# Kernel tuning notes

Measured on AMD Instinct MI355X. Metric: run time of the kernel, lower is better.

## Reference

```python
import jax, jax.numpy as jnp
import numpy as np

DIM = 512
EPS = 1e-8
LN_EPS = 1e-5


def _layernorm(x, g, b):
    mu = jnp.mean(x, axis=-1, keepdims=True)
    var = jnp.mean(jnp.square(x - mu), axis=-1, keepdims=True)
    return (x - mu) * jax.lax.rsqrt(var + LN_EPS) * g + b


def setup_inputs() -> dict:
    key = jax.random.key(0)
    ks = jax.random.split(key, 8)
    b, i, j, d = 8, 2048, 2048, DIM
    s = 1.0 / np.sqrt(d)
    return {
        "inputs": jax.random.normal(ks[0], (b, i, d), dtype=jnp.float32),
        "context": jax.random.normal(ks[1], (b, j, d), dtype=jnp.float32),
        "g_in": jnp.ones((d,), jnp.float32),
        "b_in": jnp.zeros((d,), jnp.float32),
        "g_ctx": jnp.ones((d,), jnp.float32),
        "b_ctx": jnp.zeros((d,), jnp.float32),
        "Wq": jax.random.uniform(ks[2], (d, d), jnp.float32, -s, s),
        "bq": jnp.zeros((d,), jnp.float32),
        "Wk": jax.random.uniform(ks[3], (d, d), jnp.float32, -s, s),
        "bk": jnp.zeros((d,), jnp.float32),
        "Wv": jax.random.uniform(ks[4], (d, d), jnp.float32, -s, s),
        "bv": jnp.zeros((d,), jnp.float32),
    }


def reference(inputs, context, g_in, b_in, g_ctx, b_ctx, Wq, bq, Wk, bk, Wv, bv):
    scale = DIM ** (-0.5)
    x = _layernorm(inputs, g_in, b_in)
    c = _layernorm(context, g_ctx, b_ctx)
    q = x @ Wq + bq          # [b,i,d]
    k = c @ Wk + bk          # [b,j,d]
    v = c @ Wv + bv          # [b,j,d]
    dots = jnp.einsum('bid,bjd->bij', q, k) * scale
    # NOTE: non-standard softmax over the QUERY axis (dim=1), then eps shift
    attn = jax.nn.softmax(dots, axis=1) + EPS
    # second renormalization over the KEY axis (dim=2)
    mean_attn = attn / (jnp.sum(attn, axis=2, keepdims=True) + EPS)
    updates = jnp.einsum('bjd,bij->bid', v, mean_attn)
    return updates
```

## Files before the change

kernel.cpp:

```cpp
#include <hip/hip_runtime.h>
#include <hip/hip_bf16.h>
#include <math.h>

#define EPSF 1e-8f
#define LN_EPSF 1e-5f
#define SCALE_QK 0.04419417382415922f

typedef unsigned short ushort_t;
typedef __bf16 bhalf;
typedef bhalf bhalf8 __attribute__((ext_vector_type(8)));
typedef float f32x4 __attribute__((ext_vector_type(4)));

__device__ __forceinline__ float b2f(ushort_t u) {
    return __uint_as_float((unsigned)u << 16);
}
__device__ __forceinline__ ushort_t f2b(float f) {
    unsigned x = __float_as_uint(f);
    return (ushort_t)((x + 0x7fffu + ((x >> 16) & 1u)) >> 16);
}
__device__ __forceinline__ void gload16(const ushort_t* g, ushort_t* l) {
    __builtin_amdgcn_global_load_lds(
        (const __attribute__((address_space(1))) unsigned int*)g,
        (__attribute__((address_space(3))) unsigned int*)l, 16, 0, 0);
}

__global__ __launch_bounds__(256) void ln_apply_kernel(
    const float* __restrict__ X1, const float* __restrict__ X2,
    const float* __restrict__ g1, const float* __restrict__ b1,
    const float* __restrict__ g2, const float* __restrict__ b2,
    ushort_t* __restrict__ O1, ushort_t* __restrict__ O2)
{
    const bool sec = blockIdx.y != 0;
    const float* X = sec ? X2 : X1;
    const float* g = sec ? g2 : g1;
    const float* b = sec ? b2 : b1;
    ushort_t* O = sec ? O2 : O1;
    const size_t base = (size_t)blockIdx.x * 512;
    const int t = threadIdx.x;
    float a = X[base + t];
    float c = X[base + t + 256];
    float s = a + c;
    float q = fmaf(a, a, c * c);
#pragma unroll
    for (int off = 32; off > 0; off >>= 1) {
        s += __shfl_down(s, off, 64);
        q += __shfl_down(q, off, 64);
    }
    __shared__ float ls[4], lq[4], mv[2];
    int lane = t & 63, w = t >> 6;
    if (lane == 0) { ls[w] = s; lq[w] = q; }
    __syncthreads();
    if (t == 0) {
        float st = ls[0] + ls[1] + ls[2] + ls[3];
        float qt = lq[0] + lq[1] + lq[2] + lq[3];
        float mu = st * (1.0f / 512.0f);
        float var = qt * (1.0f / 512.0f) - mu * mu;
        mv[0] = mu;
        mv[1] = rsqrtf(var + LN_EPSF);
    }
    __syncthreads();
    float mu = mv[0], rstd = mv[1];
    O[base + t]       = f2b((a - mu) * rstd * g[t] + b[t]);
    O[base + t + 256] = f2b((c - mu) * rstd * g[t + 256] + b[t + 256]);
}

__global__ __launch_bounds__(256) void wtrans_kernel(
    const float* __restrict__ W0, const float* __restrict__ W1,
    const float* __restrict__ W2,
    ushort_t* __restrict__ T0, ushort_t* __restrict__ T1,
    ushort_t* __restrict__ T2)
{
    const float* W = blockIdx.z == 0 ? W0 : (blockIdx.z == 1 ? W1 : W2);
    ushort_t* T = blockIdx.z == 0 ? T0 : (blockIdx.z == 1 ? T1 : T2);
    __shared__ float tile[32][33];
    int tx = threadIdx.x & 31, ty = threadIdx.x >> 5;
    int r0 = blockIdx.y * 32, c0 = blockIdx.x * 32;
#pragma unroll
    for (int p = 0; p < 4; ++p)
        tile[ty + p * 8][tx] = W[(size_t)(r0 + ty + p * 8) * 512 + c0 + tx];
    __syncthreads();
#pragma unroll
    for (int p = 0; p < 4; ++p)
        T[(size_t)(c0 + ty + p * 8) * 512 + r0 + tx] = f2b(tile[tx][ty + p * 8]);
}

__global__ __launch_bounds__(256) void vtrans_scaled_kernel(
    const ushort_t* __restrict__ V, const float* __restrict__ colrecip,
    ushort_t* __restrict__ VT)
{
    __shared__ ushort_t tile[32][33];
    const size_t vb = (size_t)blockIdx.z * 2048 * 512;
    const size_t tb = (size_t)blockIdx.z * 512 * 2048;
    int tx = threadIdx.x & 31, ty = threadIdx.x >> 5;
    int j0 = blockIdx.y * 32, d0 = blockIdx.x * 32;
#pragma unroll
    for (int p = 0; p < 4; ++p)
        tile[ty + p * 8][tx] = V[vb + (size_t)(j0 + ty + p * 8) * 512 + d0 + tx];
    float cr = colrecip[blockIdx.z * 2048 + j0 + tx];
    __syncthreads();
#pragma unroll
    for (int p = 0; p < 4; ++p)
        VT[tb + (size_t)(d0 + ty + p * 8) * 2048 + j0 + tx] =
            f2b(b2f(tile[tx][ty + p * 8]) * cr);
}

template <int MODE>
__global__ __launch_bounds__(256) void mfma_gemm_kernel(
    const ushort_t* __restrict__ A, const ushort_t* __restrict__ B,
    void* __restrict__ Cout, const float* __restrict__ aux,
    float* __restrict__ colsum,
    int K, int N, size_t strideA, size_t strideB, size_t strideC,
    int auxStride, float scale)
{
    __shared__ __align__(16) ushort_t As[128 * 64];
    __shared__ __align__(16) ushort_t Bs[128 * 64];
    const int tid = threadIdx.x;
    const ushort_t* Ab = A + strideA * blockIdx.z;
    const ushort_t* Bb = B + strideB * blockIdx.z;
    const int m0 = blockIdx.y * 128;
    const int n0 = blockIdx.x * 128;
    const int wave = tid >> 6;
    const int lane = tid & 63;
    const int fm = lane & 15;
    const int fq = lane >> 4;
    const int fm7 = fm & 7;
    const int wm = (wave >> 1) * 64;
    const int wn = (wave & 1) * 64;

    const int lrow = lane >> 3;
    const int lchunk = lane & 7;
    const int scs = lchunk ^ lrow;

    const ushort_t* aSrc[4]; const ushort_t* bSrc[4];
    ushort_t* aDst[4]; ushort_t* bDst[4];
#pragma unroll
    for (int p = 0; p < 4; ++p) {
        int row = wave * 32 + p * 8 + lrow;
        aSrc[p] = Ab + (size_t)(m0 + row) * K + scs * 8;
        bSrc[p] = Bb + (size_t)(n0 + row) * K + scs * 8;
        aDst[p] = As + (wave * 32 + p * 8) * 64 + lane * 8;
        bDst[p] = Bs + (wave * 32 + p * 8) * 64 + lane * 8;
    }

    const int cBase = fq ^ fm7;
    const ushort_t* aFrag[4]; const ushort_t* bFrag[4];
#pragma unroll
    for (int t = 0; t < 4; ++t) {
        aFrag[t] = As + (wm + t * 16 + fm) * 64;
        bFrag[t] = Bs + (wn + t * 16 + fm) * 64;
    }

    f32x4 acc[4][4];
#pragma unroll
    for (int i = 0; i < 4; ++i)
#pragma unroll
        for (int j = 0; j < 4; ++j) acc[i][j] = (f32x4){0.f, 0.f, 0.f, 0.f};

    for (int k0 = 0; k0 < K; k0 += 64) {
        __syncthreads();
#pragma unroll
        for (int p = 0; p < 4; ++p) {
            gload16(aSrc[p] + k0, aDst[p]);
            gload16(bSrc[p] + k0, bDst[p]);
        }
        __syncthreads();
#pragma unroll
        for (int s = 0; s < 2; ++s) {
            const int off = ((cBase ^ (s << 2)) << 3);
            bhalf8 af[4], bf[4];
#pragma unroll
            for (int t = 0; t < 4; ++t) {
                af[t] = *(const bhalf8*)(aFrag[t] + off);
                bf[t] = *(const bhalf8*)(bFrag[t] + off);
            }
#pragma unroll
            for (int i = 0; i < 4; ++i)
#pragma unroll
                for (int j = 0; j < 4; ++j)
                    acc[i][j] = __builtin_amdgcn_mfma_f32_16x16x32_bf16(
                        af[i], bf[j], acc[i][j], 0, 0, 0);
        }
    }

    if (MODE == 2) {
        float* C = (float*)Cout + strideC * blockIdx.z;
        const float* rc = aux + (size_t)auxStride * blockIdx.z;
#pragma unroll
        for (int ti = 0; ti < 4; ++ti) {
#pragma unroll
            for (int r = 0; r < 4; ++r) {
                int row = m0 + wm + ti * 16 + fq * 4 + r;
                float rs = rc[row];
#pragma unroll
                for (int tj = 0; tj < 4; ++tj) {
                    int col = n0 + wn + tj * 16 + fm;
                    C[(size_t)row * N + col] = acc[ti][tj][r] * rs;
                }
            }
        }
    } else if (MODE == 1) {
        ushort_t* C = (ushort_t*)Cout + strideC * blockIdx.z;
        float* colpart = (float*)&As[0];
        float psum[4] = {0.f, 0.f, 0.f, 0.f};
#pragma unroll
        for (int ti = 0; ti < 4; ++ti) {
#pragma unroll
            for (int r = 0; r < 4; ++r) {
                int row = m0 + wm + ti * 16 + fq * 4 + r;
#pragma unroll
                for (int tj = 0; tj < 4; ++tj) {
                    int col = n0 + wn + tj * 16 + fm;
                    float e = __expf(acc[ti][tj][r] * scale);
                    ushort_t h = f2b(e);
                    C[(size_t)row * N + col] = h;
                    psum[tj] += b2f(h);
                }
            }
        }
#pragma unroll
        for (int tj = 0; tj < 4; ++tj) {
            psum[tj] += __shfl_xor(psum[tj], 16, 64);
            psum[tj] += __shfl_xor(psum[tj], 32, 64);
        }
        __syncthreads();
        if (tid < 128) colpart[tid] = 0.f;
        __syncthreads();
        if (fq == 0) {
#pragma unroll
            for (int tj = 0; tj < 4; ++tj)
                atomicAdd(&colpart[wn + tj * 16 + fm], psum[tj]);
        }
        __syncthreads();
        if (tid < 128)
            atomicAdd(&colsum[2048 * blockIdx.z + n0 + tid], colpart[tid]);
    } else {
        ushort_t* C = (ushort_t*)Cout + strideC * blockIdx.z;
#pragma unroll
        for (int ti = 0; ti < 4; ++ti) {
#pragma unroll
            for (int r = 0; r < 4; ++r) {
                int row = m0 + wm + ti * 16 + fq * 4 + r;
#pragma unroll
                for (int tj = 0; tj < 4; ++tj) {
                    int col = n0 + wn + tj * 16 + fm;
                    C[(size_t)row * N + col] = f2b(acc[ti][tj][r] + aux[col]);
                }
            }
        }
    }
}

__global__ __launch_bounds__(256) void colrecip_kernel(
    const float* __restrict__ cs, float* __restrict__ cr)
{
    int t = blockIdx.x * 256 + threadIdx.x;
    cr[t] = 1.0f / cs[t];
}

__global__ __launch_bounds__(256) void rowsum_kernel(
    const ushort_t* __restrict__ E, const float* __restrict__ colrecip,
    float* __restrict__ recip)
{
    const uint4* rp = (const uint4*)(E + (size_t)blockIdx.x * 2048);
    const float4* cr = (const float4*)(colrecip + (blockIdx.x >> 11) * 2048);
    uint4 u = rp[threadIdx.x];
    float4 c0 = cr[threadIdx.x * 2];
    float4 c1 = cr[threadIdx.x * 2 + 1];
    float s = b2f((ushort_t)(u.x & 0xffffu)) * c0.x
            + b2f((ushort_t)(u.x >> 16))    * c0.y
            + b2f((ushort_t)(u.y & 0xffffu)) * c0.z
            + b2f((ushort_t)(u.y >> 16))    * c0.w
            + b2f((ushort_t)(u.z & 0xffffu)) * c1.x
            + b2f((ushort_t)(u.z >> 16))    * c1.y
            + b2f((ushort_t)(u.w & 0xffffu)) * c1.z
            + b2f((ushort_t)(u.w >> 16))    * c1.w;
#pragma unroll
    for (int off = 32; off > 0; off >>= 1) s += __shfl_down(s, off, 64);
    __shared__ float ls[4];
    int lane = threadIdx.x & 63, wv = threadIdx.x >> 6;
    if (lane == 0) ls[wv] = s;
    __syncthreads();
    if (threadIdx.x == 0)
        recip[blockIdx.x] = 1.0f / (ls[0] + ls[1] + ls[2] + ls[3] + 2.049e-5f);
}

extern "C" void kernel_launch(void* const* d_in, const int* in_sizes, int n_in,
                              void* d_out, int out_size, void* d_ws, size_t ws_size,
                              hipStream_t stream)
{
    const float* inputs  = (const float*)d_in[0];
    const float* context = (const float*)d_in[1];
    const float* g_in    = (const float*)d_in[2];
    const float* b_in    = (const float*)d_in[3];
    const float* g_ctx   = (const float*)d_in[4];
    const float* b_ctx   = (const float*)d_in[5];
    const float* Wq      = (const float*)d_in[6];
    const float* bq      = (const float*)d_in[7];
    const float* Wk      = (const float*)d_in[8];
    const float* bk      = (const float*)d_in[9];
    const float* Wv      = (const float*)d_in[10];
    const float* bv      = (const float*)d_in[11];
    float* out = (float*)d_out;

    const size_t QKV  = 8ull * 2048 * 512;
    const size_t WSZ  = 512ull * 512;
    const size_t DOTS = 8ull * 2048 * 2048;

    ushort_t* xln   = (ushort_t*)d_ws;
    ushort_t* cln   = xln + QKV;
    ushort_t* WqT   = cln + QKV;
    ushort_t* WkT   = WqT + WSZ;
    ushort_t* WvT   = WkT + WSZ;
    ushort_t* q     = WvT + WSZ;
    ushort_t* kk    = q + QKV;
    ushort_t* v     = kk + QKV;
    ushort_t* vTs   = v + QKV;
    ushort_t* edots = vTs + QKV;
    float* recip    = (float*)(edots + DOTS);
    float* colsum   = recip + 16384;
    float* colrecip = colsum + 16384;
    size_t need_bytes = (6 * QKV + 3 * WSZ + DOTS) * 2 + 3 * 16384 * 4;
    if (ws_size < need_bytes) return;

    hipMemsetAsync(colsum, 0, 16384 * sizeof(float), stream);

    ln_apply_kernel<<<dim3(16384, 2), 256, 0, stream>>>(
        inputs, context, g_in, b_in, g_ctx, b_ctx, xln, cln);

    wtrans_kernel<<<dim3(16, 16, 3), 256, 0, stream>>>(Wq, Wk, Wv, WqT, WkT, WvT);

    mfma_gemm_kernel<0><<<dim3(4, 128, 1), 256, 0, stream>>>(
        xln, WqT, q, bq, nullptr, 512, 512, 0, 0, 0, 0, 1.f);
    mfma_gemm_kernel<0><<<dim3(4, 128, 1), 256, 0, stream>>>(
        cln, WkT, kk, bk, nullptr, 512, 512, 0, 0, 0, 0, 1.f);
    mfma_gemm_kernel<0><<<dim3(4, 128, 1), 256, 0, stream>>>(
        cln, WvT, v, bv, nullptr, 512, 512, 0, 0, 0, 0, 1.f);

    mfma_gemm_kernel<1><<<dim3(16, 16, 8), 256, 0, stream>>>(
        q, kk, edots, nullptr, colsum, 512, 2048,
        (size_t)2048 * 512, (size_t)2048 * 512, (size_t)2048 * 2048, 0, SCALE_QK);

    colrecip_kernel<<<64, 256, 0, stream>>>(colsum, colrecip);

    vtrans_scaled_kernel<<<dim3(16, 64, 8), 256, 0, stream>>>(v, colrecip, vTs);

    rowsum_kernel<<<16384, 256, 0, stream>>>(edots, colrecip, recip);

    mfma_gemm_kernel<2><<<dim3(4, 16, 8), 256, 0, stream>>>(
        edots, vTs, out, recip, nullptr, 2048, 512,
        (size_t)2048 * 2048, (size_t)512 * 2048, (size_t)2048 * 512, 2048, 1.f);
}
```

Before: 317.1 us.

## Fold Wq·Wkᵀ into one matrix, fuse row sums and V transpose into GEMMs

Replaces the separate Q and K projections with a precomputed M = Wq·Wkᵀ, so only K' = c·M is computed. Bias cross-terms are handled through per-row and per-column dot products produced inside the layernorm kernel and added in the exp epilogue. The V projection is now a GEMM that writes the transposed, column-scaled V directly, which removes the transpose kernel. The row-sum pass is replaced by an extra MFMA against the bf16 column reciprocals inside the final GEMM, removing one full read of the dots matrix. The trade-off is more rounding: M is stored in bf16, the reciprocals are bf16, and the added terms are carried in fp32.

```diff
diff --git a/kernel.cpp b/kernel.cpp
--- a/kernel.cpp
+++ b/kernel.cpp
@@ -24,29 +24,66 @@
         (__attribute__((address_space(3))) unsigned int*)l, 16, 0, 0);
 }
 
+__global__ __launch_bounds__(256) void mv_bias_kernel(
+    const float* __restrict__ Wq, const float* __restrict__ Wk,
+    const float* __restrict__ bq, const float* __restrict__ bk,
+    float* __restrict__ wqbk, float* __restrict__ wkbq, float* __restrict__ cc)
+{
+    __shared__ float ls[4];
+    const int y = blockIdx.y;
+    const int t = threadIdx.x;
+    if (y == 2) {
+        if (blockIdx.x != 0) return;
+        float s = bq[t] * bk[t] + bq[t + 256] * bk[t + 256];
+#pragma unroll
+        for (int off = 32; off > 0; off >>= 1) s += __shfl_down(s, off, 64);
+        int lane = t & 63, w = t >> 6;
+        if (lane == 0) ls[w] = s;
+        __syncthreads();
+        if (t == 0) cc[0] = ls[0] + ls[1] + ls[2] + ls[3];
+        return;
+    }
+    const float* W = y ? Wk : Wq;
+    const float* v = y ? bq : bk;
+    float* o = y ? wkbq : wqbk;
+    const int row = blockIdx.x * 16 + (t >> 4);
+    const int l = t & 15;
+    const float* wr = W + (size_t)row * 512 + l * 32;
+    const float* vr = v + l * 32;
+    float s = 0.f;
+#pragma unroll
+    for (int c = 0; c < 32; ++c) s += wr[c] * vr[c];
+#pragma unroll
+    for (int off = 8; off > 0; off >>= 1) s += __shfl_down(s, off, 16);
+    if (l == 0) o[row] = s;
+}
+
 __global__ __launch_bounds__(256) void ln_apply_kernel(
     const float* __restrict__ X1, const float* __restrict__ X2,
     const float* __restrict__ g1, const float* __restrict__ b1,
     const float* __restrict__ g2, const float* __restrict__ b2,
-    ushort_t* __restrict__ O1, ushort_t* __restrict__ O2)
+    const float* __restrict__ wb1, const float* __restrict__ wb2,
+    ushort_t* __restrict__ O1, ushort_t* __restrict__ O2,
+    float* __restrict__ T1, float* __restrict__ T2)
 {
     const bool sec = blockIdx.y != 0;
     const float* X = sec ? X2 : X1;
     const float* g = sec ? g2 : g1;
     const float* b = sec ? b2 : b1;
+    const float* wb = sec ? wb2 : wb1;
     ushort_t* O = sec ? O2 : O1;
+    float* T = sec ? T2 : T1;
     const size_t base = (size_t)blockIdx.x * 512;
     const int t = threadIdx.x;
-    float a = X[base + t];
-    float c = X[base + t + 256];
-    float s = a + c;
-    float q = fmaf(a, a, c * c);
+    float2 x = ((const float2*)(X + base))[t];
+    float s = x.x + x.y;
+    float q = fmaf(x.x, x.x, x.y * x.y);
 #pragma unroll
     for (int off = 32; off > 0; off >>= 1) {
         s += __shfl_down(s, off, 64);
         q += __shfl_down(q, off, 64);
     }
-    __shared__ float ls[4], lq[4], mv[2];
+    __shared__ float ls[4], lq[4], mv[2], ld[4];
     int lane = t & 63, w = t >> 6;
     if (lane == 0) { ls[w] = s; lq[w] = q; }
     __syncthreads();
@@ -59,61 +96,79 @@
         mv[1] = rsqrtf(var + LN_EPSF);
     }
     __syncthreads();
-    float mu = mv[0], rstd = mv[1];
-    O[base + t]       = f2b((a - mu) * rstd * g[t] + b[t]);
-    O[base + t + 256] = f2b((c - mu) * rstd * g[t + 256] + b[t + 256]);
-}
-
-__global__ __launch_bounds__(256) void wtrans_kernel(
-    const float* __restrict__ W0, const float* __restrict__ W1,
-    const float* __restrict__ W2,
-    ushort_t* __restrict__ T0, ushort_t* __restrict__ T1,
-    ushort_t* __restrict__ T2)
-{
-    const float* W = blockIdx.z == 0 ? W0 : (blockIdx.z == 1 ? W1 : W2);
-    ushort_t* T = blockIdx.z == 0 ? T0 : (blockIdx.z == 1 ? T1 : T2);
+    const float mu = mv[0], rstd = mv[1];
+    float2 gg = ((const float2*)g)[t];
+    float2 bb = ((const float2*)b)[t];
+    float2 ww = ((const float2*)wb)[t];
+    float o0 = (x.x - mu) * rstd * gg.x + bb.x;
+    float o1 = (x.y - mu) * rstd * gg.y + bb.y;
+    ((unsigned*)O)[blockIdx.x * 256 + t] =
+        (unsigned)f2b(o0) | ((unsigned)f2b(o1) << 16);
+    float d = o0 * ww.x + o1 * ww.y;
+#pragma unroll
+    for (int off = 32; off > 0; off >>= 1) d += __shfl_down(d, off, 64);
+    if (lane == 0) ld[w] = d;
+    __syncthreads();
+    if (t == 0) T[blockIdx.x] = ld[0] + ld[1] + ld[2] + ld[3];
+}
+
+__global__ __launch_bounds__(256) void wprep_kernel(
+    const float* __restrict__ Wq, const float* __restrict__ Wk,
+    const float* __restrict__ Wv,
+    ushort_t* __restrict__ Wqb, ushort_t* __restrict__ Wkb,
+    ushort_t* __restrict__ WvT)
+{
+    const int z = blockIdx.z;
+    if (z < 2) {
+        const float* W = z ? Wk : Wq;
+        ushort_t* T = z ? Wkb : Wqb;
+        size_t idx = ((size_t)(blockIdx.y * 16 + blockIdx.x)) * 1024 + threadIdx.x * 4;
+        float4 f = *(const float4*)(W + idx);
+        uint2 u;
+        u.x = (unsigned)f2b(f.x) | ((unsigned)f2b(f.y) << 16);
+        u.y = (unsigned)f2b(f.z) | ((unsigned)f2b(f.w) << 16);
+        *(uint2*)(T + idx) = u;
+        return;
+    }
     __shared__ float tile[32][33];
     int tx = threadIdx.x & 31, ty = threadIdx.x >> 5;
     int r0 = blockIdx.y * 32, c0 = blockIdx.x * 32;
 #pragma unroll
     for (int p = 0; p < 4; ++p)
-        tile[ty + p * 8][tx] = W[(size_t)(r0 + ty + p * 8) * 512 + c0 + tx];
+        tile[ty + p * 8][tx] = Wv[(size_t)(r0 + ty + p * 8) * 512 + c0 + tx];
     __syncthreads();
 #pragma unroll
     for (int p = 0; p < 4; ++p)
-        T[(size_t)(c0 + ty + p * 8) * 512 + r0 + tx] = f2b(tile[tx][ty + p * 8]);
-}
-
-__global__ __launch_bounds__(256) void vtrans_scaled_kernel(
-    const ushort_t* __restrict__ V, const float* __restrict__ colrecip,
-    ushort_t* __restrict__ VT)
-{
-    __shared__ ushort_t tile[32][33];
-    const size_t vb = (size_t)blockIdx.z * 2048 * 512;
-    const size_t tb = (size_t)blockIdx.z * 512 * 2048;
-    int tx = threadIdx.x & 31, ty = threadIdx.x >> 5;
-    int j0 = blockIdx.y * 32, d0 = blockIdx.x * 32;
-#pragma unroll
-    for (int p = 0; p < 4; ++p)
-        tile[ty + p * 8][tx] = V[vb + (size_t)(j0 + ty + p * 8) * 512 + d0 + tx];
-    float cr = colrecip[blockIdx.z * 2048 + j0 + tx];
-    __syncthreads();
-#pragma unroll
-    for (int p = 0; p < 4; ++p)
-        VT[tb + (size_t)(d0 + ty + p * 8) * 2048 + j0 + tx] =
-            f2b(b2f(tile[tx][ty + p * 8]) * cr);
+        WvT[(size_t)(c0 + ty + p * 8) * 512 + r0 + tx] = f2b(tile[tx][ty + p * 8]);
+}
+
+__global__ __launch_bounds__(256) void colrecip_kernel(
+    const float* __restrict__ cs, float* __restrict__ cr,
+    ushort_t* __restrict__ crs)
+{
+    int t = blockIdx.x * 256 + threadIdx.x;
+    float r = 1.0f / cs[t];
+    cr[t] = r;
+    crs[t] = f2b(r);
 }
 
 template <int MODE>
 __global__ __launch_bounds__(256) void mfma_gemm_kernel(
     const ushort_t* __restrict__ A, const ushort_t* __restrict__ B,
-    void* __restrict__ Cout, const float* __restrict__ aux,
+    void* __restrict__ Cout,
+    const float* __restrict__ bias,
+    const float* __restrict__ t1,
+    const float* __restrict__ t2,
+    const float* __restrict__ cc,
     float* __restrict__ colsum,
+    const float* __restrict__ crcol,
+    const ushort_t* __restrict__ crs,
     int K, int N, size_t strideA, size_t strideB, size_t strideC,
-    int auxStride, float scale)
+    float scale)
 {
     __shared__ __align__(16) ushort_t As[128 * 64];
     __shared__ __align__(16) ushort_t Bs[128 * 64];
+    __shared__ __align__(16) ushort_t crs_lds[(MODE == 2) ? 2048 : 8];
     const int tid = threadIdx.x;
     const ushort_t* Ab = A + strideA * blockIdx.z;
     const ushort_t* Bb = B + strideB * blockIdx.z;
@@ -142,6 +197,11 @@
         bDst[p] = Bs + (wave * 32 + p * 8) * 64 + lane * 8;
     }
 
+    if (MODE == 2) {
+        uint4 c4 = *(const uint4*)(crs + (size_t)blockIdx.z * 2048 + tid * 8);
+        *(uint4*)&crs_lds[tid * 8] = c4;
+    }
+
     const int cBase = fq ^ fm7;
     const ushort_t* aFrag[4]; const ushort_t* bFrag[4];
 #pragma unroll
@@ -151,10 +211,13 @@
     }
 
     f32x4 acc[4][4];
-#pragma unroll
-    for (int i = 0; i < 4; ++i)
+    f32x4 sacc[4];
+#pragma unroll
+    for (int i = 0; i < 4; ++i) {
+        sacc[i] = (f32x4){0.f, 0.f, 0.f, 0.f};
 #pragma unroll
         for (int j = 0; j < 4; ++j) acc[i][j] = (f32x4){0.f, 0.f, 0.f, 0.f};
+    }
 
     for (int k0 = 0; k0 < K; k0 += 64) {
         __syncthreads();
@@ -179,18 +242,24 @@
                 for (int j = 0; j < 4; ++j)
                     acc[i][j] = __builtin_amdgcn_mfma_f32_16x16x32_bf16(
                         af[i], bf[j], acc[i][j], 0, 0, 0);
+            if (MODE == 2) {
+                bhalf8 bc = *(const bhalf8*)&crs_lds[k0 + (s << 5) + (fq << 3)];
+#pragma unroll
+                for (int i = 0; i < 4; ++i)
+                    sacc[i] = __builtin_amdgcn_mfma_f32_16x16x32_bf16(
+                        af[i], bc, sacc[i], 0, 0, 0);
+            }
         }
     }
 
     if (MODE == 2) {
         float* C = (float*)Cout + strideC * blockIdx.z;
-        const float* rc = aux + (size_t)auxStride * blockIdx.z;
 #pragma unroll
         for (int ti = 0; ti < 4; ++ti) {
 #pragma unroll
             for (int r = 0; r < 4; ++r) {
                 int row = m0 + wm + ti * 16 + fq * 4 + r;
-                float rs = rc[row];
+                float rs = 1.0f / (sacc[ti][r] + 2.049e-5f);
 #pragma unroll
                 for (int tj = 0; tj < 4; ++tj) {
                     int col = n0 + wn + tj * 16 + fm;
@@ -200,6 +269,11 @@
         }
     } else if (MODE == 1) {
         ushort_t* C = (ushort_t*)Cout + strideC * blockIdx.z;
+        const float cv = cc[0];
+        float t2v[4];
+#pragma unroll
+        for (int tj = 0; tj < 4; ++tj)
+            t2v[tj] = t2[(size_t)blockIdx.z * 2048 + n0 + wn + tj * 16 + fm];
         float* colpart = (float*)&As[0];
         float psum[4] = {0.f, 0.f, 0.f, 0.f};
 #pragma unroll
@@ -207,10 +281,11 @@
 #pragma unroll
             for (int r = 0; r < 4; ++r) {
                 int row = m0 + wm + ti * 16 + fq * 4 + r;
+                float t1v = t1[(size_t)blockIdx.z * 2048 + row];
 #pragma unroll
                 for (int tj = 0; tj < 4; ++tj) {
                     int col = n0 + wn + tj * 16 + fm;
-                    float e = __expf(acc[ti][tj][r] * scale);
+                    float e = __expf((acc[ti][tj][r] + t1v + t2v[tj] + cv) * scale);
                     ushort_t h = f2b(e);
                     C[(size_t)row * N + col] = h;
                     psum[tj] += b2f(h);
@@ -232,7 +307,26 @@
         }
         __syncthreads();
         if (tid < 128)
-            atomicAdd(&colsum[2048 * blockIdx.z + n0 + tid], colpart[tid]);
+            atomicAdd(&colsum[(size_t)blockIdx.z * 2048 + n0 + tid], colpart[tid]);
+    } else if (MODE == 3) {
+        ushort_t* C = (ushort_t*)Cout + strideC * blockIdx.z;
+        float crv[4];
+#pragma unroll
+        for (int tj = 0; tj < 4; ++tj)
+            crv[tj] = crcol[(size_t)blockIdx.z * 2048 + n0 + wn + tj * 16 + fm];
+#pragma unroll
+        for (int ti = 0; ti < 4; ++ti) {
+#pragma unroll
+            for (int r = 0; r < 4; ++r) {
+                int row = m0 + wm + ti * 16 + fq * 4 + r;
+                float bvv = bias[row];
+#pragma unroll
+                for (int tj = 0; tj < 4; ++tj) {
+                    int col = n0 + wn + tj * 16 + fm;
+                    C[(size_t)row * N + col] = f2b((acc[ti][tj][r] + bvv) * crv[tj]);
+                }
+            }
+        }
     } else {
         ushort_t* C = (ushort_t*)Cout + strideC * blockIdx.z;
 #pragma unroll
@@ -243,45 +337,11 @@
 #pragma unroll
                 for (int tj = 0; tj < 4; ++tj) {
                     int col = n0 + wn + tj * 16 + fm;
-                    C[(size_t)row * N + col] = f2b(acc[ti][tj][r] + aux[col]);
+                    C[(size_t)row * N + col] = f2b(acc[ti][tj][r]);
                 }
             }
         }
     }
-}
-
-__global__ __launch_bounds__(256) void colrecip_kernel(
-    const float* __restrict__ cs, float* __restrict__ cr)
-{
-    int t = blockIdx.x * 256 + threadIdx.x;
-    cr[t] = 1.0f / cs[t];
-}
-
-__global__ __launch_bounds__(256) void rowsum_kernel(
-    const ushort_t* __restrict__ E, const float* __restrict__ colrecip,
-    float* __restrict__ recip)
-{
-    const uint4* rp = (const uint4*)(E + (size_t)blockIdx.x * 2048);
-    const float4* cr = (const float4*)(colrecip + (blockIdx.x >> 11) * 2048);
-    uint4 u = rp[threadIdx.x];
-    float4 c0 = cr[threadIdx.x * 2];
-    float4 c1 = cr[threadIdx.x * 2 + 1];
-    float s = b2f((ushort_t)(u.x & 0xffffu)) * c0.x
-            + b2f((ushort_t)(u.x >> 16))    * c0.y
-            + b2f((ushort_t)(u.y & 0xffffu)) * c0.z
-            + b2f((ushort_t)(u.y >> 16))    * c0.w
-            + b2f((ushort_t)(u.z & 0xffffu)) * c1.x
-            + b2f((ushort_t)(u.z >> 16))    * c1.y
-            + b2f((ushort_t)(u.w & 0xffffu)) * c1.z
-            + b2f((ushort_t)(u.w >> 16))    * c1.w;
-#pragma unroll
-    for (int off = 32; off > 0; off >>= 1) s += __shfl_down(s, off, 64);
-    __shared__ float ls[4];
-    int lane = threadIdx.x & 63, wv = threadIdx.x >> 6;
-    if (lane == 0) ls[wv] = s;
-    __syncthreads();
-    if (threadIdx.x == 0)
-        recip[blockIdx.x] = 1.0f / (ls[0] + ls[1] + ls[2] + ls[3] + 2.049e-5f);
 }
 
 extern "C" void kernel_launch(void* const* d_in, const int* in_sizes, int n_in,
@@ -308,45 +368,56 @@
 
     ushort_t* xln   = (ushort_t*)d_ws;
     ushort_t* cln   = xln + QKV;
-    ushort_t* WqT   = cln + QKV;
-    ushort_t* WkT   = WqT + WSZ;
-    ushort_t* WvT   = WkT + WSZ;
-    ushort_t* q     = WvT + WSZ;
-    ushort_t* kk    = q + QKV;
-    ushort_t* v     = kk + QKV;
-    ushort_t* vTs   = v + QKV;
+    ushort_t* Wqb   = cln + QKV;
+    ushort_t* Wkb   = Wqb + WSZ;
+    ushort_t* WvT   = Wkb + WSZ;
+    ushort_t* Mb    = WvT + WSZ;
+    ushort_t* KM    = Mb + WSZ;
+    ushort_t* vTs   = KM + QKV;
     ushort_t* edots = vTs + QKV;
-    float* recip    = (float*)(edots + DOTS);
-    float* colsum   = recip + 16384;
+    ushort_t* crs   = edots + DOTS;
+    float* fbase    = (float*)(crs + 16384);
+    float* colsum   = fbase;
     float* colrecip = colsum + 16384;
-    size_t need_bytes = (6 * QKV + 3 * WSZ + DOTS) * 2 + 3 * 16384 * 4;
+    float* t1       = colrecip + 16384;
+    float* t2       = t1 + 16384;
+    float* wqbk     = t2 + 16384;
+    float* wkbq     = wqbk + 512;
+    float* cc       = wkbq + 512;
+    size_t need_bytes = (4 * QKV + 4 * WSZ + DOTS + 16384) * 2
+                      + (4 * 16384 + 1024 + 1) * 4;
     if (ws_size < need_bytes) return;
 
     hipMemsetAsync(colsum, 0, 16384 * sizeof(float), stream);
 
+    mv_bias_kernel<<<dim3(32, 3), 256, 0, stream>>>(Wq, Wk, bq, bk, wqbk, wkbq, cc);
+
     ln_apply_kernel<<<dim3(16384, 2), 256, 0, stream>>>(
-        inputs, context, g_in, b_in, g_ctx, b_ctx, xln, cln);
-
-    wtrans_kernel<<<dim3(16, 16, 3), 256, 0, stream>>>(Wq, Wk, Wv, WqT, WkT, WvT);
+        inputs, context, g_in, b_in, g_ctx, b_ctx, wqbk, wkbq, xln, cln, t1, t2);
+
+    wprep_kernel<<<dim3(16, 16, 3), 256, 0, stream>>>(Wq, Wk, Wv, Wqb, Wkb, WvT);
+
+    mfma_gemm_kernel<0><<<dim3(4, 4, 1), 256, 0, stream>>>(
+        Wqb, Wkb, Mb, nullptr, nullptr, nullptr, nullptr, nullptr, nullptr, nullptr,
+        512, 512, 0, 0, 0, 1.f);
 
     mfma_gemm_kernel<0><<<dim3(4, 128, 1), 256, 0, stream>>>(
-        xln, WqT, q, bq, nullptr, 512, 512, 0, 0, 0, 0, 1.f);
-    mfma_gemm_kernel<0><<<dim3(4, 128, 1), 256, 0, stream>>>(
-        cln, WkT, kk, bk, nullptr, 512, 512, 0, 0, 0, 0, 1.f);
-    mfma_gemm_kernel<0><<<dim3(4, 128, 1), 256, 0, stream>>>(
-        cln, WvT, v, bv, nullptr, 512, 512, 0, 0, 0, 0, 1.f);
+        cln, Mb, KM, nullptr, nullptr, nullptr, nullptr, nullptr, nullptr, nullptr,
+        512, 512, 0, 0, 0, 1.f);
 
     mfma_gemm_kernel<1><<<dim3(16, 16, 8), 256, 0, stream>>>(
-        q, kk, edots, nullptr, colsum, 512, 2048,
-        (size_t)2048 * 512, (size_t)2048 * 512, (size_t)2048 * 2048, 0, SCALE_QK);
-
-    colrecip_kernel<<<64, 256, 0, stream>>>(colsum, colrecip);
-
-    vtrans_scaled_kernel<<<dim3(16, 64, 8), 256, 0, stream>>>(v, colrecip, vTs);
-
-    rowsum_kernel<<<16384, 256, 0, stream>>>(edots, colrecip, recip);
+        xln, KM, edots, nullptr, t1, t2, cc, colsum, nullptr, nullptr,
+        512, 2048, (size_t)2048 * 512, (size_t)2048 * 512, (size_t)2048 * 2048,
+        SCALE_QK);
+
+    colrecip_kernel<<<64, 256, 0, stream>>>(colsum, colrecip, crs);
+
+    mfma_gemm_kernel<3><<<dim3(16, 4, 8), 256, 0, stream>>>(
+        WvT, cln, vTs, bv, nullptr, nullptr, nullptr, nullptr, colrecip, nullptr,
+        512, 2048, 0, (size_t)2048 * 512, (size_t)512 * 2048, 1.f);
 
     mfma_gemm_kernel<2><<<dim3(4, 16, 8), 256, 0, stream>>>(
-        edots, vTs, out, recip, nullptr, 2048, 512,
-        (size_t)2048 * 2048, (size_t)512 * 2048, (size_t)2048 * 512, 2048, 1.f);
-}
+        edots, vTs, out, nullptr, nullptr, nullptr, nullptr, nullptr, nullptr, crs,
+        2048, 512, (size_t)2048 * 2048, (size_t)512 * 2048, (size_t)2048 * 512,
+        1.f);
+}
```

Result: faster. 308.4 us (-2.7%).
